# Kernel tuning notes

Hardware: AMD Instinct MI355X
Metric: run time of the kernel (lower is better)

Reference implementation:

```python
import jax, jax.numpy as jnp
import numpy as np

D_MODEL = 1024
NUM_HEADS = 16
D_K = D_MODEL // NUM_HEADS


def setup_inputs() -> dict:
    key = jax.random.key(0)
    k1, k2, k3, k4, k5 = jax.random.split(key, 5)
    x = jax.random.normal(k1, (2, 2048, D_MODEL), dtype=jnp.float32)
    s = 1.0 / np.sqrt(D_MODEL)
    W_q = jax.random.normal(k2, (D_MODEL, D_MODEL), dtype=jnp.float32) * s
    W_k = jax.random.normal(k3, (D_MODEL, D_MODEL), dtype=jnp.float32) * s
    W_v = jax.random.normal(k4, (D_MODEL, D_MODEL), dtype=jnp.float32) * s
    W_o = jax.random.normal(k5, (D_MODEL, D_MODEL), dtype=jnp.float32) * s
    return {"x": x, "W_q": W_q, "W_k": W_k, "W_v": W_v, "W_o": W_o}


def reference(x, W_q, W_k, W_v, W_o):
    B, S, _ = x.shape
    # projections (nn.Linear: y = x @ W.T); split heads -> (B, H, S, d_k)
    def split_heads(y):
        return y.reshape(B, S, NUM_HEADS, D_K).transpose(0, 2, 1, 3)
    Q = split_heads(x @ W_q.T)
    K = split_heads(x @ W_k.T)
    V = split_heads(x @ W_v.T)
    scale = 1.0 / jnp.sqrt(jnp.asarray(D_K, dtype=x.dtype))
    scores = jnp.einsum("bhqd,bhkd->bhqk", Q, K) * scale  # (B,H,S,S)
    causal = jnp.triu(jnp.ones((S, S), dtype=bool), k=1)
    scores = jnp.where(causal, -jnp.inf, scores)
    attn = jax.nn.softmax(scores, axis=-1)
    out = jnp.einsum("bhqk,bhkd->bhqd", attn, V)
    out = out.transpose(0, 2, 1, 3).reshape(B, S, D_MODEL)
    return out @ W_o.T
```

## Files before the change

kernel.cpp:

```cpp
#include <hip/hip_runtime.h>
#include <hip/hip_bf16.h>

typedef __bf16 bf16x8 __attribute__((ext_vector_type(8)));
typedef float f32x4 __attribute__((ext_vector_type(4)));
typedef float f32x16 __attribute__((ext_vector_type(16)));
typedef unsigned short ushort_t;
typedef unsigned int uint2v __attribute__((ext_vector_type(2)));

#define DEVI __device__ __forceinline__

static constexpr int KDIM = 1024;
static constexpr int SEQ  = 2048;

DEVI ushort_t f2bf(float f) {
  union { float f; unsigned u; } a; a.f = f;
  unsigned u = a.u;
  return (ushort_t)((u + 0x7FFFu + ((u >> 16) & 1u)) >> 16);
}

DEVI unsigned cvtpk(float lo, float hi) {
  unsigned r;
  asm("v_cvt_pk_bf16_f32 %0, %1, %2" : "=v"(r) : "v"(lo), "v"(hi));
  return r;
}

DEVI uint2v plswap(unsigned a, unsigned b) {
  return __builtin_amdgcn_permlane32_swap(a, b, 0, 0);
}
DEVI float swap_max(float x) {
  union { float f; unsigned u; } a; a.f = x;
  const uint2v r = plswap(a.u, a.u);
  union { unsigned u; float f; } p0, p1; p0.u = r[0]; p1.u = r[1];
  return fmaxf(p0.f, p1.f);
}
DEVI float swap_sum(float x) {
  union { float f; unsigned u; } a; a.f = x;
  const uint2v r = plswap(a.u, a.u);
  union { unsigned u; float f; } p0, p1; p0.u = r[0]; p1.u = r[1];
  return p0.f + p1.f;
}

DEVI void gload16(const ushort_t* g, ushort_t* l) {
  __builtin_amdgcn_global_load_lds(
      (const __attribute__((address_space(1))) void*)g,
      (__attribute__((address_space(3))) void*)l,
      16, 0, 0);
}

__global__ void cast_all(const float* __restrict__ x,
                         const float* __restrict__ w0, const float* __restrict__ w1,
                         const float* __restrict__ w2, const float* __restrict__ w3,
                         ushort_t* __restrict__ xb, ushort_t* __restrict__ wb) {
  const int i = blockIdx.x * 256 + threadIdx.x;
  float4 v; ushort_t* dst; int idx;
  if (i < (1 << 20)) {
    v = ((const float4*)x)[i]; dst = xb; idx = i;
  } else {
    const int j = i - (1 << 20);
    const int which = j >> 18;
    const float* w = which == 0 ? w0 : which == 1 ? w1 : which == 2 ? w2 : w3;
    v = ((const float4*)w)[j & 262143]; dst = wb; idx = j;
  }
  ushort4 o;
  o.x = f2bf(v.x); o.y = f2bf(v.y); o.z = f2bf(v.z); o.w = f2bf(v.w);
  ((ushort4*)dst)[idx] = o;
}

DEVI void stage_half(const ushort_t* __restrict__ G, int rowbase, int kcol,
                     ushort_t* lbase, int tid) {
#pragma unroll
  for (int rd = 0; rd < 2; ++rd) {
    const int row = rd * 128 + (tid >> 2), cg = tid & 3;
    const int gcol = kcol + ((cg ^ ((row >> 1) & 3)) << 3);
    gload16(G + (size_t)(rowbase + row) * 1024 + gcol, lbase + row * 32 + cg * 8);
  }
}

__global__ __launch_bounds__(512, 2) void gemm256_qkv(const ushort_t* __restrict__ xb,
                                                      const ushort_t* __restrict__ wb,
                                                      ushort_t* __restrict__ qfo,
                                                      ushort_t* __restrict__ kfo,
                                                      ushort_t* __restrict__ vfo) {
  __shared__ ushort_t sm[2][2][2][8192];
  const int tid = threadIdx.x;
  const int wid = tid >> 6, l = tid & 63;
  const int wm = wid >> 2, wn = wid & 3;
  const int lg = l >> 4, ll = l & 15;
  const int orig = blockIdx.x;
  const int wg = (orig & 7) * 24 + (orig >> 3);

  int m0, n0;
  const ushort_t *Ap, *Bp;
  bool isV;
  if (wg < 128) {
    m0 = (wg >> 4) * 256;
    n0 = (wg & 15) * 256;
    Ap = wb; Bp = xb; isV = false;
  } else {
    const int lo = wg - 128;
    m0 = (lo >> 2) * 256;
    n0 = (lo & 3) * 256;
    Ap = xb; Bp = wb + (size_t)2048 * 1024; isV = true;
  }

  f32x4 acc[8][4];
#pragma unroll
  for (int i = 0; i < 8; ++i)
#pragma unroll
    for (int j = 0; j < 4; ++j) acc[i][j] = f32x4{0.f, 0.f, 0.f, 0.f};

#define STG(T, MAT, KH) do { if ((T) < 16) \
    stage_half((MAT) ? Bp : Ap, (MAT) ? n0 : m0, (T) * 64 + (KH) * 32, \
               &sm[(T) & 1][MAT][KH][0], tid); } while (0)
#define BARX do { asm volatile("" ::: "memory"); __builtin_amdgcn_s_barrier(); \
                  asm volatile("" ::: "memory"); } while (0)
#define PHASE(P, KH, MH, STG_STMT, WAIT_STMT) do {                              \
    bf16x8 af_[4], bf_[4];                                                      \
    _Pragma("unroll")                                                           \
    for (int mr = 0; mr < 4; ++mr) {                                            \
      const int ra = wm * 128 + ((MH) * 4 + mr) * 16 + ll;                      \
      af_[mr] = *(const bf16x8*)&sm[P][0][KH][ra * 32 + ((lg ^ ((ra >> 1) & 3)) << 3)]; \
    }                                                                           \
    _Pragma("unroll")                                                           \
    for (int nr = 0; nr < 4; ++nr) {                                            \
      const int rb = wn * 64 + nr * 16 + ll;                                    \
      bf_[nr] = *(const bf16x8*)&sm[P][1][KH][rb * 32 + ((lg ^ ((rb >> 1) & 3)) << 3)]; \
    }                                                                           \
    STG_STMT;                                                                   \
    BARX;                                                                       \
    __builtin_amdgcn_s_setprio(1);                                              \
    _Pragma("unroll")                                                           \
    for (int mr = 0; mr < 4; ++mr)                                              \
      _Pragma("unroll")                                                         \
      for (int nr = 0; nr < 4; ++nr)                                            \
        acc[(MH) * 4 + mr][nr] = __builtin_amdgcn_mfma_f32_16x16x32_bf16(       \
            af_[mr], bf_[nr], acc[(MH) * 4 + mr][nr], 0, 0, 0);                 \
    __builtin_amdgcn_s_setprio(0);                                              \
    WAIT_STMT;                                                                  \
    BARX;                                                                       \
  } while (0)
#define WAIT4 asm volatile("s_waitcnt vmcnt(4)" ::: "memory")
#define WAIT0 asm volatile("s_waitcnt vmcnt(0)" ::: "memory")

  STG(0, 0, 0); STG(0, 1, 0); STG(0, 0, 1); STG(0, 1, 1); STG(1, 0, 0); STG(1, 1, 0);
  WAIT4;
  BARX;

  for (int I = 0; I < 7; ++I) {
    const int T = 2 * I;
    PHASE(0, 0, 0, STG(T + 1, 0, 1), );
    PHASE(0, 0, 1, STG(T + 1, 1, 1), );
    PHASE(0, 1, 0, STG(T + 2, 0, 0), );
    PHASE(0, 1, 1, STG(T + 2, 1, 0), WAIT4);
    PHASE(1, 0, 0, STG(T + 2, 0, 1), );
    PHASE(1, 0, 1, STG(T + 2, 1, 1), );
    PHASE(1, 1, 0, STG(T + 3, 0, 0), );
    PHASE(1, 1, 1, STG(T + 3, 1, 0), WAIT4);
  }
  PHASE(0, 0, 0, STG(15, 0, 1), );
  PHASE(0, 0, 1, STG(15, 1, 1), );
  PHASE(0, 1, 0, , );
  PHASE(0, 1, 1, , WAIT0);
  PHASE(1, 0, 0, , );
  PHASE(1, 0, 1, , );
  PHASE(1, 1, 0, , );
  PHASE(1, 1, 1, , );

#undef STG
#undef PHASE
#undef WAIT4
#undef WAIT0
#undef BARX

  if (!isV) {
    const int whichK = m0 >> 10;
    const int lgh = lg >> 1, lgb = lg & 1;
    ushort_t* const dstb = whichK ? kfo : qfo;
#pragma unroll
    for (int mr = 0; mr < 8; ++mr) {
      const int dout = (m0 & 1023) + wm * 128 + mr * 16;
      const int h = dout >> 6;
      const int ks = (dout >> 4) & 3;
#pragma unroll
      for (int nr = 0; nr < 4; ++nr) {
        const int s = n0 + wn * 64 + nr * 16 + ll;
        const int b = s >> 11, s2 = s & 2047;
        const size_t bh = (size_t)(b * 16 + h);
        size_t addr;
        if (whichK == 0)
          addr = ((bh * 64 + (s2 >> 5)) * 4 + ks) * 512 + (lgh * 32 + (s2 & 31)) * 8 + lgb * 4;
        else
          addr = ((bh * 32 + (s2 >> 6)) * 8 + ((s2 >> 5) & 1) * 4 + ks) * 512 +
                 (lgh * 32 + (s2 & 31)) * 8 + lgb * 4;
        const unsigned u0 = cvtpk(acc[mr][nr][0], acc[mr][nr][1]);
        const unsigned u1 = cvtpk(acc[mr][nr][2], acc[mr][nr][3]);
        *(uint2v*)(dstb + addr) = uint2v{u0, u1};
      }
    }
  } else {
#pragma unroll
    for (int mr = 0; mr < 8; ++mr) {
#pragma unroll
      for (int nr = 0; nr < 4; ++nr) {
        const int gm0 = m0 + wm * 128 + mr * 16 + 4 * lg;
        const int gn = n0 + wn * 64 + nr * 16 + ll;
        const int h = gn >> 6, d = gn & 63;
        const int b = gm0 >> 11, s0 = gm0 & 2047;
        const size_t bh = (size_t)(b * 16 + h);
        const size_t base = ((bh * 32 + (s0 >> 6)) * 8 + (d >> 5) * 4 + ((s0 >> 4) & 3)) * 512 +
                            (((s0 >> 3) & 1) * 32 + (d & 31)) * 8 + (s0 & 7);
        const unsigned u0 = cvtpk(acc[mr][nr][0], acc[mr][nr][1]);
        const unsigned u1 = cvtpk(acc[mr][nr][2], acc[mr][nr][3]);
        *(uint2v*)(vfo + base) = uint2v{u0, u1};
      }
    }
  }
}

__global__ __launch_bounds__(256, 3) void gemm_out(const ushort_t* __restrict__ A,
                                                   const ushort_t* __restrict__ Bm,
                                                   float* __restrict__ ofp) {
  __shared__ ushort_t smA[128 * 64];
  __shared__ ushort_t smB[128 * 64];
  const int tid = threadIdx.x;
  const int w = tid >> 6, l = tid & 63;
  const int lg = l >> 4, ll = l & 15;
  const int lr = l >> 3, lc = (l & 7) * 8;
  const int m0 = blockIdx.y * 128, n0 = blockIdx.x * 128;
  const int wm = (w >> 1) * 64, wn = (w & 1) * 64;

  f32x4 acc[4][4];
#pragma unroll
  for (int i = 0; i < 4; ++i)
#pragma unroll
    for (int j = 0; j < 4; ++j) acc[i][j] = f32x4{0.f, 0.f, 0.f, 0.f};

  for (int k0 = 0; k0 < KDIM; k0 += 64) {
    __syncthreads();
#pragma unroll
    for (int i = 0; i < 4; ++i) {
      const int ci = w * 4 + i;
      gload16(A  + (size_t)(m0 + ci * 8 + lr) * KDIM + k0 + lc, smA + ci * 512);
      gload16(Bm + (size_t)(n0 + ci * 8 + lr) * KDIM + k0 + lc, smB + ci * 512);
    }
    __syncthreads();
#pragma unroll
    for (int ks = 0; ks < 2; ++ks) {
      bf16x8 af[4], bfr[4];
#pragma unroll
      for (int t = 0; t < 4; ++t) {
        af[t]  = *(const bf16x8*)(smA + (wm + t * 16 + ll) * 64 + ks * 32 + lg * 8);
        bfr[t] = *(const bf16x8*)(smB + (wn + t * 16 + ll) * 64 + ks * 32 + lg * 8);
      }
      __builtin_amdgcn_s_setprio(1);
#pragma unroll
      for (int i = 0; i < 4; ++i)
#pragma unroll
        for (int j = 0; j < 4; ++j)
          acc[i][j] = __builtin_amdgcn_mfma_f32_16x16x32_bf16(af[i], bfr[j], acc[i][j], 0, 0, 0);
      __builtin_amdgcn_s_setprio(0);
    }
  }

#pragma unroll
  for (int i = 0; i < 4; ++i)
#pragma unroll
    for (int j = 0; j < 4; ++j) {
      const int gm0 = m0 + wm + i * 16 + 4 * lg;
      const int gn = n0 + wn + j * 16 + ll;
#pragma unroll
      for (int r = 0; r < 4; ++r)
        ofp[(size_t)(gm0 + r) * 1024 + gn] = acc[i][j][r];
    }
}

__global__ __launch_bounds__(256, 2) void attn_fwd(const ushort_t* __restrict__ Qf,
                                                   const ushort_t* __restrict__ Kf,
                                                   const ushort_t* __restrict__ Vf,
                                                   ushort_t* __restrict__ ao) {
  const int tid = threadIdx.x;
  const int w = tid >> 6, l = tid & 63;
  const int l31 = l & 31, hi = l >> 5;
  const int bh = blockIdx.y;
  const int qx = ((bh >> 4) & 1) ? (15 - (int)blockIdx.x) : (int)blockIdx.x;
  const int q0 = qx * 128;
  const int q = q0 + w * 32 + l31;

  const ushort_t* Qw = Qf + ((size_t)bh * 64 + (q0 >> 5) + w) * 4 * 512 + l * 8;
  const ushort_t* Kb = Kf + (size_t)bh * 32 * 8 * 512 + l * 8;
  const ushort_t* Vb = Vf + (size_t)bh * 32 * 8 * 512 + l * 8;

  bf16x8 qf[4];
#pragma unroll
  for (int ks = 0; ks < 4; ++ks)
    qf[ks] = *(const bf16x8*)(Qw + ks * 512);

  f32x16 oT[2];
#pragma unroll
  for (int dh = 0; dh < 2; ++dh)
#pragma unroll
    for (int r = 0; r < 16; ++r) oT[dh][r] = 0.f;
  float mi = -3.0e38f, li = 0.f;

  const float SCL2 = 0.18033688011112042f;
  const int myNkt = (q0 + 32 * w + 31) / 64 + 1;

  bf16x8 kf[8];
#pragma unroll
  for (int f = 0; f < 8; ++f) kf[f] = *(const bf16x8*)(Kb + f * 512);

  for (int kt = 0; kt < myNkt; ++kt) {
    const ushort_t* Vt_ = Vb + (size_t)kt * 8 * 512;
    bf16x8 vf[8];
#pragma unroll
    for (int f = 0; f < 8; ++f) vf[f] = *(const bf16x8*)(Vt_ + f * 512);

    f32x16 sc[2];
#pragma unroll
    for (int h2 = 0; h2 < 2; ++h2)
#pragma unroll
      for (int r = 0; r < 16; ++r) sc[h2][r] = 0.f;
    __builtin_amdgcn_s_setprio(1);
#pragma unroll
    for (int h2 = 0; h2 < 2; ++h2)
#pragma unroll
      for (int ks = 0; ks < 4; ++ks)
        sc[h2] = __builtin_amdgcn_mfma_f32_32x32x16_bf16(kf[h2 * 4 + ks], qf[ks], sc[h2], 0, 0, 0);
    __builtin_amdgcn_s_setprio(0);

    const bool more = (kt + 1 < myNkt);
    bf16x8 kfn[8];
    if (more) {
      const ushort_t* Kt_ = Kb + (size_t)(kt + 1) * 8 * 512;
#pragma unroll
      for (int f = 0; f < 8; ++f) kfn[f] = *(const bf16x8*)(Kt_ + f * 512);
    }

    if (kt == myNkt - 1) {
      const int thr0 = q - kt * 64 - 4 * hi;
#pragma unroll
      for (int r = 0; r < 16; ++r) {
        const int cr = (r & 3) + 8 * (r >> 2);
        if (cr > thr0)      sc[0][r] = -3.0e38f;
        if (cr > thr0 - 32) sc[1][r] = -3.0e38f;
      }
    }

    float t8[8];
#pragma unroll
    for (int r = 0; r < 8; ++r)
      t8[r] = fmaxf(fmaxf(sc[0][r], sc[0][r + 8]), fmaxf(sc[1][r], sc[1][r + 8]));
    float mx = fmaxf(fmaxf(fmaxf(t8[0], t8[1]), fmaxf(t8[2], t8[3])),
                     fmaxf(fmaxf(t8[4], t8[5]), fmaxf(t8[6], t8[7])));
    mx = swap_max(mx);

    if (!__all(mx <= mi + 44.0f)) {
      const float mnew = fmaxf(mi, mx);
      const float al = __builtin_amdgcn_exp2f((mi - mnew) * SCL2);
      li *= al;
#pragma unroll
      for (int dh = 0; dh < 2; ++dh)
#pragma unroll
        for (int r = 0; r < 16; ++r) oT[dh][r] *= al;
      mi = mnew;
    }

    const float ms = mi * SCL2;
#pragma unroll
    for (int h2 = 0; h2 < 2; ++h2)
#pragma unroll
      for (int r = 0; r < 16; ++r)
        sc[h2][r] = __builtin_amdgcn_exp2f(__builtin_fmaf(sc[h2][r], SCL2, -ms));
    float s8[8];
#pragma unroll
    for (int r = 0; r < 8; ++r)
      s8[r] = (sc[0][r] + sc[0][r + 8]) + (sc[1][r] + sc[1][r + 8]);
    float sum = ((s8[0] + s8[1]) + (s8[2] + s8[3])) + ((s8[4] + s8[5]) + (s8[6] + s8[7]));
    li += swap_sum(sum);

    bf16x8 pf[4];
#pragma unroll
    for (int m = 0; m < 4; ++m) {
      const int H = m >> 1, base = (m & 1) * 8;
      const unsigned a0 = cvtpk(sc[H][base + 0], sc[H][base + 1]);
      const unsigned a1 = cvtpk(sc[H][base + 2], sc[H][base + 3]);
      const unsigned a2 = cvtpk(sc[H][base + 4], sc[H][base + 5]);
      const unsigned a3 = cvtpk(sc[H][base + 6], sc[H][base + 7]);
      const uint2v r02 = plswap(a0, a2);
      const uint2v r13 = plswap(a1, a3);
      union { unsigned u[4]; bf16x8 v; } cv;
      cv.u[0] = r02[0]; cv.u[1] = r13[0]; cv.u[2] = r02[1]; cv.u[3] = r13[1];
      pf[m] = cv.v;
    }

    __builtin_amdgcn_s_setprio(1);
#pragma unroll
    for (int dh = 0; dh < 2; ++dh)
#pragma unroll
      for (int m = 0; m < 4; ++m)
        oT[dh] = __builtin_amdgcn_mfma_f32_32x32x16_bf16(vf[dh * 4 + m], pf[m], oT[dh], 0, 0, 0);
    __builtin_amdgcn_s_setprio(0);

    if (more) {
#pragma unroll
      for (int f = 0; f < 8; ++f) kf[f] = kfn[f];
    }
  }

  const float inv = 1.f / li;
  const int b = bh >> 4, h = bh & 15;
  ushort_t* orow = ao + ((size_t)b * 2048 + q) * 1024 + h * 64;
#pragma unroll
  for (int dh = 0; dh < 2; ++dh)
#pragma unroll
    for (int rg = 0; rg < 4; ++rg) {
      const unsigned u0 = cvtpk(oT[dh][4 * rg + 0] * inv, oT[dh][4 * rg + 1] * inv);
      const unsigned u1 = cvtpk(oT[dh][4 * rg + 2] * inv, oT[dh][4 * rg + 3] * inv);
      *(uint2v*)(orow + dh * 32 + hi * 4 + rg * 8) = uint2v{u0, u1};
    }
}

extern "C" void kernel_launch(void* const* d_in, const int* in_sizes, int n_in,
                              void* d_out, int out_size, void* d_ws, size_t ws_size,
                              hipStream_t stream) {
  (void)in_sizes; (void)n_in; (void)out_size; (void)ws_size;
  const float* x  = (const float*)d_in[0];
  const float* wq = (const float*)d_in[1];
  const float* wk = (const float*)d_in[2];
  const float* wv = (const float*)d_in[3];
  const float* wo = (const float*)d_in[4];

  char* ws = (char*)d_ws;
  ushort_t* xb  = (ushort_t*)ws;
  ushort_t* wb  = (ushort_t*)(ws + (8u  << 20));
  ushort_t* qf  = (ushort_t*)(ws + (16u << 20));
  ushort_t* kf  = (ushort_t*)(ws + (24u << 20));
  ushort_t* vf  = (ushort_t*)(ws + (40u << 20));
  ushort_t* ao  = xb;
  float* out = (float*)d_out;

  cast_all   <<<8192, 256, 0, stream>>>(x, wq, wk, wv, wo, xb, wb);
  gemm256_qkv<<<192, 512, 0, stream>>>(xb, wb, qf, kf, vf);
  attn_fwd   <<<dim3(16, 32), 256, 0, stream>>>(qf, kf, vf, ao);
  gemm_out   <<<dim3(8, 32), 256, 0, stream>>>(ao, wb + 3 * 1048576, out);
}
```

Before: 170.4 us.

## Process two query tiles per wave in attention to reuse K/V fragments

Each attention block now runs 2 waves instead of 4, and each wave handles two 32-row query tiles (rows qA and qA+64) that share the same K and V register fragments loaded from global memory. This halves K/V global loads per query row and interleaves two independent MFMA chains. The A tile finishes one key tile earlier and the B tile gets an extra tail iteration with masking. Register pressure roughly doubles for accumulators, which may lower occupancy or cause spills, and there are fewer waves per block to hide latency.

```diff
diff --git a/kernel.cpp b/kernel.cpp
--- a/kernel.cpp
+++ b/kernel.cpp
@@ -274,7 +274,65 @@
     }
 }
 
-__global__ __launch_bounds__(256, 2) void attn_fwd(const ushort_t* __restrict__ Qf,
+DEVI void sm_pack(f32x16* sc, float& mi, float& li, f32x16* oT, bf16x8* pf) {
+  const float SCL2 = 0.18033688011112042f;
+  float t8[8];
+#pragma unroll
+  for (int r = 0; r < 8; ++r)
+    t8[r] = fmaxf(fmaxf(sc[0][r], sc[0][r + 8]), fmaxf(sc[1][r], sc[1][r + 8]));
+  float mx = fmaxf(fmaxf(fmaxf(t8[0], t8[1]), fmaxf(t8[2], t8[3])),
+                   fmaxf(fmaxf(t8[4], t8[5]), fmaxf(t8[6], t8[7])));
+  mx = swap_max(mx);
+
+  if (!__all(mx <= mi + 44.0f)) {
+    const float mnew = fmaxf(mi, mx);
+    const float al = __builtin_amdgcn_exp2f((mi - mnew) * SCL2);
+    li *= al;
+#pragma unroll
+    for (int dh = 0; dh < 2; ++dh)
+#pragma unroll
+      for (int r = 0; r < 16; ++r) oT[dh][r] *= al;
+    mi = mnew;
+  }
+
+  const float ms = mi * SCL2;
+#pragma unroll
+  for (int h2 = 0; h2 < 2; ++h2)
+#pragma unroll
+    for (int r = 0; r < 16; ++r)
+      sc[h2][r] = __builtin_amdgcn_exp2f(__builtin_fmaf(sc[h2][r], SCL2, -ms));
+  float s8[8];
+#pragma unroll
+  for (int r = 0; r < 8; ++r)
+    s8[r] = (sc[0][r] + sc[0][r + 8]) + (sc[1][r] + sc[1][r + 8]);
+  float sum = ((s8[0] + s8[1]) + (s8[2] + s8[3])) + ((s8[4] + s8[5]) + (s8[6] + s8[7]));
+  li += swap_sum(sum);
+
+#pragma unroll
+  for (int m = 0; m < 4; ++m) {
+    const int H = m >> 1, base = (m & 1) * 8;
+    const unsigned a0 = cvtpk(sc[H][base + 0], sc[H][base + 1]);
+    const unsigned a1 = cvtpk(sc[H][base + 2], sc[H][base + 3]);
+    const unsigned a2 = cvtpk(sc[H][base + 4], sc[H][base + 5]);
+    const unsigned a3 = cvtpk(sc[H][base + 6], sc[H][base + 7]);
+    const uint2v r02 = plswap(a0, a2);
+    const uint2v r13 = plswap(a1, a3);
+    union { unsigned u[4]; bf16x8 v; } cv;
+    cv.u[0] = r02[0]; cv.u[1] = r13[0]; cv.u[2] = r02[1]; cv.u[3] = r13[1];
+    pf[m] = cv.v;
+  }
+}
+
+DEVI void mask_tile(f32x16* sc, int thr0) {
+#pragma unroll
+  for (int r = 0; r < 16; ++r) {
+    const int cr = (r & 3) + 8 * (r >> 2);
+    if (cr > thr0)      sc[0][r] = -3.0e38f;
+    if (cr > thr0 - 32) sc[1][r] = -3.0e38f;
+  }
+}
+
+__global__ __launch_bounds__(128, 2) void attn_fwd(const ushort_t* __restrict__ Qf,
                                                    const ushort_t* __restrict__ Kf,
                                                    const ushort_t* __restrict__ Vf,
                                                    ushort_t* __restrict__ ao) {
@@ -284,139 +342,128 @@
   const int bh = blockIdx.y;
   const int qx = ((bh >> 4) & 1) ? (15 - (int)blockIdx.x) : (int)blockIdx.x;
   const int q0 = qx * 128;
-  const int q = q0 + w * 32 + l31;
-
-  const ushort_t* Qw = Qf + ((size_t)bh * 64 + (q0 >> 5) + w) * 4 * 512 + l * 8;
+  const int qA = q0 + w * 32 + l31;
+  const int qB = qA + 64;
+
   const ushort_t* Kb = Kf + (size_t)bh * 32 * 8 * 512 + l * 8;
   const ushort_t* Vb = Vf + (size_t)bh * 32 * 8 * 512 + l * 8;
-
-  bf16x8 qf[4];
-#pragma unroll
-  for (int ks = 0; ks < 4; ++ks)
-    qf[ks] = *(const bf16x8*)(Qw + ks * 512);
-
-  f32x16 oT[2];
+  const ushort_t* QwA = Qf + ((size_t)bh * 64 + (q0 >> 5) + w) * 4 * 512 + l * 8;
+  const ushort_t* QwB = QwA + 2 * 4 * 512;
+
+  bf16x8 qfA[4], qfB[4];
+#pragma unroll
+  for (int ks = 0; ks < 4; ++ks) {
+    qfA[ks] = *(const bf16x8*)(QwA + ks * 512);
+    qfB[ks] = *(const bf16x8*)(QwB + ks * 512);
+  }
+
+  f32x16 oTA[2], oTB[2];
 #pragma unroll
   for (int dh = 0; dh < 2; ++dh)
 #pragma unroll
-    for (int r = 0; r < 16; ++r) oT[dh][r] = 0.f;
-  float mi = -3.0e38f, li = 0.f;
-
-  const float SCL2 = 0.18033688011112042f;
-  const int myNkt = (q0 + 32 * w + 31) / 64 + 1;
+    for (int r = 0; r < 16; ++r) { oTA[dh][r] = 0.f; oTB[dh][r] = 0.f; }
+  float miA = -3.0e38f, liA = 0.f, miB = -3.0e38f, liB = 0.f;
+
+  const int nA = 2 * qx + 1;
 
   bf16x8 kf[8];
 #pragma unroll
   for (int f = 0; f < 8; ++f) kf[f] = *(const bf16x8*)(Kb + f * 512);
 
-  for (int kt = 0; kt < myNkt; ++kt) {
+  for (int kt = 0; kt < nA; ++kt) {
     const ushort_t* Vt_ = Vb + (size_t)kt * 8 * 512;
     bf16x8 vf[8];
 #pragma unroll
     for (int f = 0; f < 8; ++f) vf[f] = *(const bf16x8*)(Vt_ + f * 512);
 
-    f32x16 sc[2];
+    f32x16 scA[2], scB[2];
 #pragma unroll
     for (int h2 = 0; h2 < 2; ++h2)
 #pragma unroll
-      for (int r = 0; r < 16; ++r) sc[h2][r] = 0.f;
+      for (int r = 0; r < 16; ++r) { scA[h2][r] = 0.f; scB[h2][r] = 0.f; }
     __builtin_amdgcn_s_setprio(1);
 #pragma unroll
     for (int h2 = 0; h2 < 2; ++h2)
 #pragma unroll
+      for (int ks = 0; ks < 4; ++ks) {
+        scA[h2] = __builtin_amdgcn_mfma_f32_32x32x16_bf16(kf[h2 * 4 + ks], qfA[ks], scA[h2], 0, 0, 0);
+        scB[h2] = __builtin_amdgcn_mfma_f32_32x32x16_bf16(kf[h2 * 4 + ks], qfB[ks], scB[h2], 0, 0, 0);
+      }
+    __builtin_amdgcn_s_setprio(0);
+
+    const ushort_t* Kt_ = Kb + (size_t)(kt + 1) * 8 * 512;
+    bf16x8 kfn[8];
+#pragma unroll
+    for (int f = 0; f < 8; ++f) kfn[f] = *(const bf16x8*)(Kt_ + f * 512);
+
+    if (kt == nA - 1) mask_tile(scA, qA - kt * 64 - 4 * hi);
+
+    bf16x8 pfA[4], pfB[4];
+    sm_pack(scA, miA, liA, oTA, pfA);
+    sm_pack(scB, miB, liB, oTB, pfB);
+
+    __builtin_amdgcn_s_setprio(1);
+#pragma unroll
+    for (int dh = 0; dh < 2; ++dh)
+#pragma unroll
+      for (int m = 0; m < 4; ++m) {
+        oTA[dh] = __builtin_amdgcn_mfma_f32_32x32x16_bf16(vf[dh * 4 + m], pfA[m], oTA[dh], 0, 0, 0);
+        oTB[dh] = __builtin_amdgcn_mfma_f32_32x32x16_bf16(vf[dh * 4 + m], pfB[m], oTB[dh], 0, 0, 0);
+      }
+    __builtin_amdgcn_s_setprio(0);
+
+#pragma unroll
+    for (int f = 0; f < 8; ++f) kf[f] = kfn[f];
+  }
+
+  {
+    const int kt = nA;
+    const ushort_t* Vt_ = Vb + (size_t)kt * 8 * 512;
+    bf16x8 vf[8];
+#pragma unroll
+    for (int f = 0; f < 8; ++f) vf[f] = *(const bf16x8*)(Vt_ + f * 512);
+
+    f32x16 scB[2];
+#pragma unroll
+    for (int h2 = 0; h2 < 2; ++h2)
+#pragma unroll
+      for (int r = 0; r < 16; ++r) scB[h2][r] = 0.f;
+    __builtin_amdgcn_s_setprio(1);
+#pragma unroll
+    for (int h2 = 0; h2 < 2; ++h2)
+#pragma unroll
       for (int ks = 0; ks < 4; ++ks)
-        sc[h2] = __builtin_amdgcn_mfma_f32_32x32x16_bf16(kf[h2 * 4 + ks], qf[ks], sc[h2], 0, 0, 0);
+        scB[h2] = __builtin_amdgcn_mfma_f32_32x32x16_bf16(kf[h2 * 4 + ks], qfB[ks], scB[h2], 0, 0, 0);
     __builtin_amdgcn_s_setprio(0);
 
-    const bool more = (kt + 1 < myNkt);
-    bf16x8 kfn[8];
-    if (more) {
-      const ushort_t* Kt_ = Kb + (size_t)(kt + 1) * 8 * 512;
-#pragma unroll
-      for (int f = 0; f < 8; ++f) kfn[f] = *(const bf16x8*)(Kt_ + f * 512);
-    }
-
-    if (kt == myNkt - 1) {
-      const int thr0 = q - kt * 64 - 4 * hi;
-#pragma unroll
-      for (int r = 0; r < 16; ++r) {
-        const int cr = (r & 3) + 8 * (r >> 2);
-        if (cr > thr0)      sc[0][r] = -3.0e38f;
-        if (cr > thr0 - 32) sc[1][r] = -3.0e38f;
-      }
-    }
-
-    float t8[8];
-#pragma unroll
-    for (int r = 0; r < 8; ++r)
-      t8[r] = fmaxf(fmaxf(sc[0][r], sc[0][r + 8]), fmaxf(sc[1][r], sc[1][r + 8]));
-    float mx = fmaxf(fmaxf(fmaxf(t8[0], t8[1]), fmaxf(t8[2], t8[3])),
-                     fmaxf(fmaxf(t8[4], t8[5]), fmaxf(t8[6], t8[7])));
-    mx = swap_max(mx);
-
-    if (!__all(mx <= mi + 44.0f)) {
-      const float mnew = fmaxf(mi, mx);
-      const float al = __builtin_amdgcn_exp2f((mi - mnew) * SCL2);
-      li *= al;
-#pragma unroll
-      for (int dh = 0; dh < 2; ++dh)
-#pragma unroll
-        for (int r = 0; r < 16; ++r) oT[dh][r] *= al;
-      mi = mnew;
-    }
-
-    const float ms = mi * SCL2;
-#pragma unroll
-    for (int h2 = 0; h2 < 2; ++h2)
-#pragma unroll
-      for (int r = 0; r < 16; ++r)
-        sc[h2][r] = __builtin_amdgcn_exp2f(__builtin_fmaf(sc[h2][r], SCL2, -ms));
-    float s8[8];
-#pragma unroll
-    for (int r = 0; r < 8; ++r)
-      s8[r] = (sc[0][r] + sc[0][r + 8]) + (sc[1][r] + sc[1][r + 8]);
-    float sum = ((s8[0] + s8[1]) + (s8[2] + s8[3])) + ((s8[4] + s8[5]) + (s8[6] + s8[7]));
-    li += swap_sum(sum);
-
-    bf16x8 pf[4];
-#pragma unroll
-    for (int m = 0; m < 4; ++m) {
-      const int H = m >> 1, base = (m & 1) * 8;
-      const unsigned a0 = cvtpk(sc[H][base + 0], sc[H][base + 1]);
-      const unsigned a1 = cvtpk(sc[H][base + 2], sc[H][base + 3]);
-      const unsigned a2 = cvtpk(sc[H][base + 4], sc[H][base + 5]);
-      const unsigned a3 = cvtpk(sc[H][base + 6], sc[H][base + 7]);
-      const uint2v r02 = plswap(a0, a2);
-      const uint2v r13 = plswap(a1, a3);
-      union { unsigned u[4]; bf16x8 v; } cv;
-      cv.u[0] = r02[0]; cv.u[1] = r13[0]; cv.u[2] = r02[1]; cv.u[3] = r13[1];
-      pf[m] = cv.v;
-    }
+    mask_tile(scB, qB - kt * 64 - 4 * hi);
+
+    bf16x8 pfB[4];
+    sm_pack(scB, miB, liB, oTB, pfB);
 
     __builtin_amdgcn_s_setprio(1);
 #pragma unroll
     for (int dh = 0; dh < 2; ++dh)
 #pragma unroll
       for (int m = 0; m < 4; ++m)
-        oT[dh] = __builtin_amdgcn_mfma_f32_32x32x16_bf16(vf[dh * 4 + m], pf[m], oT[dh], 0, 0, 0);
+        oTB[dh] = __builtin_amdgcn_mfma_f32_32x32x16_bf16(vf[dh * 4 + m], pfB[m], oTB[dh], 0, 0, 0);
     __builtin_amdgcn_s_setprio(0);
-
-    if (more) {
-#pragma unroll
-      for (int f = 0; f < 8; ++f) kf[f] = kfn[f];
-    }
-  }
-
-  const float inv = 1.f / li;
+  }
+
   const int b = bh >> 4, h = bh & 15;
-  ushort_t* orow = ao + ((size_t)b * 2048 + q) * 1024 + h * 64;
+  const float invA = 1.f / liA, invB = 1.f / liB;
+  ushort_t* orowA = ao + ((size_t)b * 2048 + qA) * 1024 + h * 64;
+  ushort_t* orowB = ao + ((size_t)b * 2048 + qB) * 1024 + h * 64;
 #pragma unroll
   for (int dh = 0; dh < 2; ++dh)
 #pragma unroll
     for (int rg = 0; rg < 4; ++rg) {
-      const unsigned u0 = cvtpk(oT[dh][4 * rg + 0] * inv, oT[dh][4 * rg + 1] * inv);
-      const unsigned u1 = cvtpk(oT[dh][4 * rg + 2] * inv, oT[dh][4 * rg + 3] * inv);
-      *(uint2v*)(orow + dh * 32 + hi * 4 + rg * 8) = uint2v{u0, u1};
+      const unsigned a0 = cvtpk(oTA[dh][4 * rg + 0] * invA, oTA[dh][4 * rg + 1] * invA);
+      const unsigned a1 = cvtpk(oTA[dh][4 * rg + 2] * invA, oTA[dh][4 * rg + 3] * invA);
+      *(uint2v*)(orowA + dh * 32 + hi * 4 + rg * 8) = uint2v{a0, a1};
+      const unsigned b0 = cvtpk(oTB[dh][4 * rg + 0] * invB, oTB[dh][4 * rg + 1] * invB);
+      const unsigned b1 = cvtpk(oTB[dh][4 * rg + 2] * invB, oTB[dh][4 * rg + 3] * invB);
+      *(uint2v*)(orowB + dh * 32 + hi * 4 + rg * 8) = uint2v{b0, b1};
     }
 }
 
@@ -441,6 +488,6 @@
 
   cast_all   <<<8192, 256, 0, stream>>>(x, wq, wk, wv, wo, xb, wb);
   gemm256_qkv<<<192, 512, 0, stream>>>(xb, wb, qf, kf, vf);
-  attn_fwd   <<<dim3(16, 32), 256, 0, stream>>>(qf, kf, vf, ao);
+  attn_fwd   <<<dim3(16, 32), 128, 0, stream>>>(qf, kf, vf, ao);
   gemm_out   <<<dim3(8, 32), 256, 0, stream>>>(ao, wb + 3 * 1048576, out);
 }
```

Result: slower. 187.9 us (+10.2%).
